# Kernel optimization log

Hardware: AMD Instinct MI355X
Metric: run time of the kernel (lower is better)

## Reference

```python
import jax, jax.numpy as jnp
import numpy as np

B, S, H, P = 8, 2048, 256, 64
NQ = 20

def setup_inputs() -> dict:
    key = jax.random.key(0)
    ks = jax.random.split(key, 12)
    s = lambda fan_in: 1.0 / np.sqrt(fan_in)
    return {
        "feature_x": jax.random.normal(ks[0], (B, S, H), dtype=jnp.float32),
        "param_x": jax.random.normal(ks[1], (B, S, P), dtype=jnp.float32),
        "sim_w1": jax.random.uniform(ks[2], (H, H // 2), jnp.float32, -s(H), s(H)),
        "sim_b1": jax.random.uniform(ks[3], (H // 2,), jnp.float32, -s(H), s(H)),
        "sim_w2": jax.random.uniform(ks[4], (H // 2, 1), jnp.float32, -s(H // 2), s(H // 2)),
        "sim_b2": jax.random.uniform(ks[5], (1,), jnp.float32, -s(H // 2), s(H // 2)),
        "conf_w1": jax.random.uniform(ks[6], (H, H // 2), jnp.float32, -s(H), s(H)),
        "conf_b1": jax.random.uniform(ks[7], (H // 2,), jnp.float32, -s(H), s(H)),
        "conf_w2": jax.random.uniform(ks[8], (H // 2, 1), jnp.float32, -s(H // 2), s(H // 2)),
        "conf_b2": jax.random.uniform(ks[9], (1,), jnp.float32, -s(H // 2), s(H // 2)),
        "questions": jax.random.randint(ks[10], (B, S), 0, NQ, dtype=jnp.int64 if jax.config.jax_enable_x64 else jnp.int32),
    }

def _mlp_scalar(x, w1, b1, w2, b2):
    # [B,S,H] -> [B,S] (dropout is eval-mode identity)
    h = jax.nn.relu(jnp.einsum("bsh,hk->bsk", x, w1) + b1)
    return (jnp.einsum("bsk,ko->bso", h, w2) + b2)[..., 0]

def reference(feature_x, param_x, sim_w1, sim_b1, sim_w2, sim_b2,
              conf_w1, conf_b1, conf_w2, conf_b2, questions):
    similarities = _mlp_scalar(feature_x, sim_w1, sim_b1, sim_w2, sim_b2)          # [B,S]
    confidences = jax.nn.sigmoid(_mlp_scalar(feature_x, conf_w1, conf_b1, conf_w2, conf_b2))  # [B,S]
    # multiplicative equality mask (zeros, not -inf, outside group — faithful to source)
    qmask = (questions[:, :, None] == questions[:, None, :]).astype(feature_x.dtype)  # [B,S,S]
    logits = similarities[:, :, None] * qmask                                        # [B,i,j]
    attn = jax.nn.softmax(logits, axis=-2)                                           # softmax over i
    smoothed = jnp.einsum("bij,bip->bjp", attn, param_x)                              # attn^T @ param_x
    c = confidences[..., None]
    return c * param_x + (1.0 - c) * smoothed
```

## Files before the change

### kernel.cpp

```cpp
#include <hip/hip_runtime.h>
#include <math.h>

#define B_  8
#define S_  2048
#define H_  256
#define HK_ 128
#define P_  64
#define NQ_ 20
#define M_  (B_*S_)
#define ACC_STRIDE 2688

#define WS_SIM   0
#define WS_CONF  16384
#define WS_ACC   32768
#define WS_WT    54272

typedef __attribute__((ext_vector_type(8))) short bf16x8;
typedef __attribute__((ext_vector_type(4))) float f32x4;

__global__ void prep_kernel(const float* __restrict__ sw1, const float* __restrict__ cw1,
                            short* __restrict__ wt, float* __restrict__ ws_acc)
{
    const int t = blockIdx.x * 256 + threadIdx.x;
    const int k = t & 255, n = (t >> 8) & 127, mlp = t >> 15;
    const float* w1 = mlp ? cw1 : sw1;
    union { float f; unsigned u; } c; c.f = w1[k * HK_ + n];
    unsigned r = (c.u + 0x7FFF + ((c.u >> 16) & 1)) >> 16;
    wt[t] = (short)r;
    if (t < B_ * ACC_STRIDE) ws_acc[t] = 0.f;
}

__launch_bounds__(256)
__global__ void mlp_mfma_kernel(const float* __restrict__ fx, const short* __restrict__ wt,
                                const float* __restrict__ sb1, const float* __restrict__ sw2,
                                const float* __restrict__ sb2, const float* __restrict__ cb1,
                                const float* __restrict__ cw2, const float* __restrict__ cb2,
                                float* __restrict__ sim, float* __restrict__ conf)
{
    __shared__ short lds[2 * 128 * 72];
    const int tid  = threadIdx.x;
    const int w    = tid >> 6, l = tid & 63;
    const int col  = l & 15, quad = l >> 4;
    const int mlp  = w >> 1, mt = w & 1;
    const int row  = blockIdx.x * 32 + mt * 16 + col;

    f32x4 acc[8];
    #pragma unroll
    for (int nt = 0; nt < 8; ++nt) acc[nt] = (f32x4){0.f, 0.f, 0.f, 0.f};

    const float* fxrow = fx + (size_t)row * H_;

    for (int ch = 0; ch < 4; ++ch) {
        __syncthreads();
        #pragma unroll
        for (int i = 0; i < 8; ++i) {
            int u  = tid + 256 * i;
            int um = u >> 10, un = (u >> 3) & 127, us = u & 7;
            const short* src = wt + um * 32768 + un * 256 + ch * 64 + us * 8;
            *(uint4*)&lds[um * 9216 + un * 72 + us * 8] = *(const uint4*)src;
        }
        __syncthreads();
        #pragma unroll
        for (int ks = 0; ks < 2; ++ks) {
            const int kg = ch * 64 + ks * 32 + quad * 8;
            float4 a0 = *(const float4*)(fxrow + kg);
            float4 a1 = *(const float4*)(fxrow + kg + 4);
            float af[8] = {a0.x, a0.y, a0.z, a0.w, a1.x, a1.y, a1.z, a1.w};
            bf16x8 ahi, alo;
            #pragma unroll
            for (int i = 0; i < 8; ++i) {
                union { float f; unsigned u; } c; c.f = af[i];
                unsigned hi = c.u >> 16;
                ahi[i] = (short)hi;
                union { float f; unsigned u; } h2; h2.u = hi << 16;
                union { float f; unsigned u; } c2; c2.f = af[i] - h2.f;
                alo[i] = (short)(c2.u >> 16);
            }
            const short* bbase = lds + mlp * 9216 + ks * 32 + quad * 8;
            #pragma unroll
            for (int nt = 0; nt < 8; ++nt) {
                bf16x8 bf = *(const bf16x8*)(bbase + (nt * 16 + col) * 72);
                acc[nt] = __builtin_amdgcn_mfma_f32_16x16x32_bf16(ahi, bf, acc[nt], 0, 0, 0);
                acc[nt] = __builtin_amdgcn_mfma_f32_16x16x32_bf16(alo, bf, acc[nt], 0, 0, 0);
            }
        }
    }

    const float* b1 = mlp ? cb1 : sb1;
    const float* w2 = mlp ? cw2 : sw2;
    const float  b2v = mlp ? cb2[0] : sb2[0];
    float p[4] = {0.f, 0.f, 0.f, 0.f};
    #pragma unroll
    for (int nt = 0; nt < 8; ++nt) {
        float b1c = b1[nt * 16 + col];
        float w2c = w2[nt * 16 + col];
        #pragma unroll
        for (int j = 0; j < 4; ++j)
            p[j] += fmaxf(acc[nt][j] + b1c, 0.f) * w2c;
    }
    #pragma unroll
    for (int off = 8; off >= 1; off >>= 1)
        #pragma unroll
        for (int j = 0; j < 4; ++j) p[j] += __shfl_down(p[j], off, 16);

    if (col == 0) {
        #pragma unroll
        for (int j = 0; j < 4; ++j) {
            int r = blockIdx.x * 32 + mt * 16 + quad * 4 + j;
            float v = p[j] + b2v;
            if (mlp == 0) sim[r] = v;
            else          conf[r] = 1.0f / (1.0f + expf(-v));
        }
    }
}

__launch_bounds__(256)
__global__ void accum_kernel(const float* __restrict__ sim, const int* __restrict__ questions,
                             const float* __restrict__ px, float* __restrict__ ws_acc)
{
    const int b = blockIdx.x;
    const int chunk = blockIdx.y;
    const int tid = threadIdx.x;
    const int lane = tid & 63;
    const int g = tid >> 6;
    __shared__ float accs[4][ACC_STRIDE];
    for (int s = tid; s < 4 * ACC_STRIDE; s += 256) ((float*)accs)[s] = 0.f;
    __syncthreads();

    const float* simb = sim + b * S_;
    const int*   qb   = questions + b * S_;
    const float* pxb  = px + (size_t)b * S_ * P_;

    float Treg = 0.f;
    const int i0 = chunk * 64 + g;
    for (int t = 0; t < 16; ++t) {
        int i = i0 + 4 * t;
        int qi = qb[i];
        float e = expf(simb[i]);
        float v = pxb[(size_t)i * P_ + lane];
        Treg += v;
        accs[g][qi * 64 + lane]        += v;
        accs[g][(20 + qi) * 64 + lane] += e * v;
        if (lane == 0) {
            accs[g][2624 + qi] += e;
            accs[g][2644 + qi] += 1.0f;
        }
    }
    accs[g][2560 + lane] += Treg;
    __syncthreads();

    float* dst = ws_acc + (size_t)b * ACC_STRIDE;
    for (int s = tid; s < ACC_STRIDE; s += 256) {
        float sum = accs[0][s] + accs[1][s] + accs[2][s] + accs[3][s];
        atomicAdd(dst + s, sum);
    }
}

__global__ void output_kernel(const float* __restrict__ px, const float* __restrict__ conf,
                              const int* __restrict__ questions, const float* __restrict__ ws_acc,
                              float* __restrict__ out)
{
    const int idx = blockIdx.x * 256 + threadIdx.x;
    const int row = idx >> 4;
    const int p4  = idx & 15;
    const int b   = row >> 11;
    const float c = conf[row];
    const int   q = questions[row];
    const float* accb = ws_acc + (size_t)b * ACC_STRIDE;
    const float4 T = *(const float4*)(accb + 2560 + p4 * 4);
    const float4 G = *(const float4*)(accb + q * 64 + p4 * 4);
    const float4 E = *(const float4*)(accb + (20 + q) * 64 + p4 * 4);
    const float denom = ((float)S_ - accb[2644 + q]) + accb[2624 + q];
    const float inv = 1.0f / denom;
    const float4 pv = ((const float4*)px)[idx];
    const float om = 1.0f - c;
    float4 o;
    o.x = c * pv.x + om * ((T.x - G.x + E.x) * inv);
    o.y = c * pv.y + om * ((T.y - G.y + E.y) * inv);
    o.z = c * pv.z + om * ((T.z - G.z + E.z) * inv);
    o.w = c * pv.w + om * ((T.w - G.w + E.w) * inv);
    ((float4*)out)[idx] = o;
}

extern "C" void kernel_launch(void* const* d_in, const int* in_sizes, int n_in,
                              void* d_out, int out_size, void* d_ws, size_t ws_size,
                              hipStream_t stream) {
    const float* fx  = (const float*)d_in[0];
    const float* px  = (const float*)d_in[1];
    const float* sw1 = (const float*)d_in[2];
    const float* sb1 = (const float*)d_in[3];
    const float* sw2 = (const float*)d_in[4];
    const float* sb2 = (const float*)d_in[5];
    const float* cw1 = (const float*)d_in[6];
    const float* cb1 = (const float*)d_in[7];
    const float* cw2 = (const float*)d_in[8];
    const float* cb2 = (const float*)d_in[9];
    const int* questions = (const int*)d_in[10];
    float* out = (float*)d_out;

    float* ws     = (float*)d_ws;
    float* sim    = ws + WS_SIM;
    float* conf   = ws + WS_CONF;
    float* ws_acc = ws + WS_ACC;
    short* wt     = (short*)(ws + WS_WT);

    prep_kernel<<<256, 256, 0, stream>>>(sw1, cw1, wt, ws_acc);
    mlp_mfma_kernel<<<M_ / 32, 256, 0, stream>>>(fx, wt, sb1, sw2, sb2,
                                                 cb1, cw2, cb2, sim, conf);
    accum_kernel<<<dim3(B_, 32), 256, 0, stream>>>(sim, questions, px, ws_acc);
    output_kernel<<<(M_ * P_ / 4) / 256, 256, 0, stream>>>(px, conf, questions,
                                                           ws_acc, out);
}
```

Baseline: 117.7 us.

## Pre-swizzle MLP weights into MFMA fragment order and drop LDS staging

The prep kernel now writes the bf16 first-layer weights directly in per-lane MFMA B-fragment order. The MLP kernel then loads each fragment with one 16-byte global load, with no LDS tile copies or block barriers. This removes shared-memory staging and synchronization. In exchange every wave re-reads 64KB of weights from cache, and the prep kernel runs with fewer blocks.

New measurement: 109.9 us, median of 2. 1.07x faster.

```diff
diff --git a/kernel.cpp b/kernel.cpp
--- a/kernel.cpp
+++ b/kernel.cpp
@@ -19,25 +19,31 @@
 typedef __attribute__((ext_vector_type(4))) float f32x4;
 
 __global__ void prep_kernel(const float* __restrict__ sw1, const float* __restrict__ cw1,
-                            short* __restrict__ wt, float* __restrict__ ws_acc)
+                            short* __restrict__ wtf, float* __restrict__ ws_acc)
 {
     const int t = blockIdx.x * 256 + threadIdx.x;
-    const int k = t & 255, n = (t >> 8) & 127, mlp = t >> 15;
+    const int l = t & 63, nt = (t >> 6) & 7, kt = (t >> 9) & 7, mlp = t >> 12;
+    const int col = l & 15, quad = l >> 4;
+    const int n = nt * 16 + col;
     const float* w1 = mlp ? cw1 : sw1;
-    union { float f; unsigned u; } c; c.f = w1[k * HK_ + n];
-    unsigned r = (c.u + 0x7FFF + ((c.u >> 16) & 1)) >> 16;
-    wt[t] = (short)r;
-    if (t < B_ * ACC_STRIDE) ws_acc[t] = 0.f;
+    short frag[8];
+    #pragma unroll
+    for (int j = 0; j < 8; ++j) {
+        int k = kt * 32 + quad * 8 + j;
+        union { float f; unsigned u; } c; c.f = w1[k * HK_ + n];
+        frag[j] = (short)((c.u + 0x7FFF + ((c.u >> 16) & 1)) >> 16);
+    }
+    *(uint4*)(wtf + (size_t)t * 8) = *(const uint4*)frag;
+    for (int s = t; s < B_ * ACC_STRIDE; s += 8192) ws_acc[s] = 0.f;
 }
 
 __launch_bounds__(256)
-__global__ void mlp_mfma_kernel(const float* __restrict__ fx, const short* __restrict__ wt,
+__global__ void mlp_mfma_kernel(const float* __restrict__ fx, const short* __restrict__ wtf,
                                 const float* __restrict__ sb1, const float* __restrict__ sw2,
                                 const float* __restrict__ sb2, const float* __restrict__ cb1,
                                 const float* __restrict__ cw2, const float* __restrict__ cb2,
                                 float* __restrict__ sim, float* __restrict__ conf)
 {
-    __shared__ short lds[2 * 128 * 72];
     const int tid  = threadIdx.x;
     const int w    = tid >> 6, l = tid & 63;
     const int col  = l & 15, quad = l >> 4;
@@ -49,40 +55,29 @@
     for (int nt = 0; nt < 8; ++nt) acc[nt] = (f32x4){0.f, 0.f, 0.f, 0.f};
 
     const float* fxrow = fx + (size_t)row * H_;
-
-    for (int ch = 0; ch < 4; ++ch) {
-        __syncthreads();
+    const short* wf = wtf + (size_t)mlp * 32768 + (size_t)l * 8;
+
+    #pragma unroll
+    for (int kt = 0; kt < 8; ++kt) {
+        float4 a0 = *(const float4*)(fxrow + kt * 32 + quad * 8);
+        float4 a1 = *(const float4*)(fxrow + kt * 32 + quad * 8 + 4);
+        float af[8] = {a0.x, a0.y, a0.z, a0.w, a1.x, a1.y, a1.z, a1.w};
+        bf16x8 ahi, alo;
         #pragma unroll
         for (int i = 0; i < 8; ++i) {
-            int u  = tid + 256 * i;
-            int um = u >> 10, un = (u >> 3) & 127, us = u & 7;
-            const short* src = wt + um * 32768 + un * 256 + ch * 64 + us * 8;
-            *(uint4*)&lds[um * 9216 + un * 72 + us * 8] = *(const uint4*)src;
-        }
-        __syncthreads();
-        #pragma unroll
-        for (int ks = 0; ks < 2; ++ks) {
-            const int kg = ch * 64 + ks * 32 + quad * 8;
-            float4 a0 = *(const float4*)(fxrow + kg);
-            float4 a1 = *(const float4*)(fxrow + kg + 4);
-            float af[8] = {a0.x, a0.y, a0.z, a0.w, a1.x, a1.y, a1.z, a1.w};
-            bf16x8 ahi, alo;
-            #pragma unroll
-            for (int i = 0; i < 8; ++i) {
-                union { float f; unsigned u; } c; c.f = af[i];
-                unsigned hi = c.u >> 16;
-                ahi[i] = (short)hi;
-                union { float f; unsigned u; } h2; h2.u = hi << 16;
-                union { float f; unsigned u; } c2; c2.f = af[i] - h2.f;
-                alo[i] = (short)(c2.u >> 16);
-            }
-            const short* bbase = lds + mlp * 9216 + ks * 32 + quad * 8;
-            #pragma unroll
-            for (int nt = 0; nt < 8; ++nt) {
-                bf16x8 bf = *(const bf16x8*)(bbase + (nt * 16 + col) * 72);
-                acc[nt] = __builtin_amdgcn_mfma_f32_16x16x32_bf16(ahi, bf, acc[nt], 0, 0, 0);
-                acc[nt] = __builtin_amdgcn_mfma_f32_16x16x32_bf16(alo, bf, acc[nt], 0, 0, 0);
-            }
+            union { float f; unsigned u; } c; c.f = af[i];
+            unsigned hi = c.u >> 16;
+            ahi[i] = (short)hi;
+            union { float f; unsigned u; } h2; h2.u = hi << 16;
+            union { float f; unsigned u; } c2; c2.f = af[i] - h2.f;
+            alo[i] = (short)(c2.u >> 16);
+        }
+        const short* base = wf + (size_t)kt * 4096;
+        #pragma unroll
+        for (int nt = 0; nt < 8; ++nt) {
+            bf16x8 bf = *(const bf16x8*)(base + nt * 512);
+            acc[nt] = __builtin_amdgcn_mfma_f32_16x16x32_bf16(ahi, bf, acc[nt], 0, 0, 0);
+            acc[nt] = __builtin_amdgcn_mfma_f32_16x16x32_bf16(alo, bf, acc[nt], 0, 0, 0);
         }
     }
 
@@ -202,10 +197,10 @@
     float* sim    = ws + WS_SIM;
     float* conf   = ws + WS_CONF;
     float* ws_acc = ws + WS_ACC;
-    short* wt     = (short*)(ws + WS_WT);
-
-    prep_kernel<<<256, 256, 0, stream>>>(sw1, cw1, wt, ws_acc);
-    mlp_mfma_kernel<<<M_ / 32, 256, 0, stream>>>(fx, wt, sb1, sw2, sb2,
+    short* wtf    = (short*)(ws + WS_WT);
+
+    prep_kernel<<<32, 256, 0, stream>>>(sw1, cw1, wtf, ws_acc);
+    mlp_mfma_kernel<<<M_ / 32, 256, 0, stream>>>(fx, wtf, sb1, sw2, sb2,
                                                  cb1, cw2, cb2, sim, conf);
     accum_kernel<<<dim3(B_, 32), 256, 0, stream>>>(sim, questions, px, ws_acc);
     output_kernel<<<(M_ * P_ / 4) / 256, 256, 0, stream>>>(px, conf, questions,
```
